# Kernel tuning notes

Measured on AMD Instinct MI355X. Metric: run time of the kernel, lower is better.

The kernel has to match this reference:

```python
import jax, jax.numpy as jnp
import numpy as np

D_IN = 2
D_Q = 8
N_TOKEN = 512
FPD = 64            # fre_per_dim = (N_TOKEN*D_Q)**(1/D_IN)
FRE_UB = 10.0
FFN_MULT = 4
N_ATTN = 4
N_MLP = 2           # n_total_blocks - n_attn_blocks
B = 8192
EPS_LN = 1e-5
EPS_SIG = 1e-8


def _ln(x, g, b):
    m = jnp.mean(x, axis=-1, keepdims=True)
    v = jnp.var(x, axis=-1, keepdims=True)
    return (x - m) * jax.lax.rsqrt(v + EPS_LN) * g + b


def _rff_buffers():
    # freqs: linspace(0, fre_ub, FPD+1)[1:]
    f = jnp.linspace(0.0, FRE_UB, FPD + 1)[1:]
    # cartesian_prod(f, f): first factor varies slowest
    grid = jnp.stack(jnp.meshgrid(f, f, indexing='ij'), axis=-1).reshape(-1, D_IN)
    omega_raw = grid.reshape(N_TOKEN, D_Q, D_IN)
    G = omega_raw[..., -1]                                 # [T, d_q]
    f_min = G.min(axis=-1, keepdims=True)
    f_max = G.max(axis=-1, keepdims=True)
    G = (G - f_min) / (f_max - f_min + EPS_SIG) * 2.0 - 1.0
    omega = omega_raw * jnp.sqrt(jnp.asarray(2.0 / (D_Q * N_TOKEN), jnp.float32))
    phase = jnp.linspace(0.0, 2.0 * np.pi, N_TOKEN * D_Q).reshape(1, N_TOKEN, D_Q)
    return omega.astype(jnp.float32), G.astype(jnp.float32), phase.astype(jnp.float32)


def setup_inputs() -> dict:
    key = jax.random.key(0)
    ks = iter(jax.random.split(key, 64))
    T, F = N_TOKEN, FFN_MULT * N_TOKEN
    s = 0.02

    def w(shape):
        return (jax.random.normal(next(ks), shape, jnp.float32) * s)

    omega, G, phase = _rff_buffers()
    inp = {
        'x': jax.random.normal(next(ks), (B, D_IN), jnp.float32),
        'omega': omega, 'G': G, 'phase': phase,
        'l1_w': w((T, D_IN)), 'l1_b': jnp.zeros((T,), jnp.float32),
        # attention blocks (stacked over N_ATTN)
        'mu_w': w((N_ATTN, T, T)), 'mu_b': jnp.zeros((N_ATTN, T), jnp.float32),
        'sg_w': w((N_ATTN, T, T)), 'sg_b': jnp.zeros((N_ATTN, T), jnp.float32),
        'aln_q_g': jnp.ones((N_ATTN, T), jnp.float32), 'aln_q_b': jnp.zeros((N_ATTN, T), jnp.float32),
        'aln_f_g': jnp.ones((N_ATTN, T), jnp.float32), 'aln_f_b': jnp.zeros((N_ATTN, T), jnp.float32),
        'a_w1': w((N_ATTN, F, T)), 'a_b1': jnp.zeros((N_ATTN, F), jnp.float32),
        'a_w2': w((N_ATTN, T, F)), 'a_b2': jnp.zeros((N_ATTN, T), jnp.float32),
        # MLP blocks (stacked over N_MLP)
        'mln_g': jnp.ones((N_MLP, T), jnp.float32), 'mln_b': jnp.zeros((N_MLP, T), jnp.float32),
        'm_w1': w((N_MLP, F, T)), 'm_b1': jnp.zeros((N_MLP, F), jnp.float32),
        'm_w2': w((N_MLP, T, F)), 'm_b2': jnp.zeros((N_MLP, T), jnp.float32),
        'ro_w': w((1, T)), 'ro_b': jnp.zeros((1,), jnp.float32),
    }
    return inp


def reference(x, omega, G, phase, l1_w, l1_b, mu_w, mu_b, sg_w, sg_b,
              aln_q_g, aln_q_b, aln_f_g, aln_f_b, a_w1, a_b1, a_w2, a_b2,
              mln_g, mln_b, m_w1, m_b1, m_w2, m_b2, ro_w, ro_b):
    # RFF tokenizer: H[b,n,k] = cos(omega[n,k,:] . x[b,:] + phase)
    H = jnp.cos(jnp.einsum('nkd,bd->bnk', omega, x) + phase)   # [B,T,d_q]
    Q = jax.nn.silu(x @ l1_w.T + l1_b)                          # [B,T]
    for i in range(N_ATTN):
        q = _ln(Q, aln_q_g[i], aln_q_b[i])
        mu = jnp.tanh(q @ mu_w[i].T + mu_b[i])[..., None]       # [B,T,1]
        sig = (q @ sg_w[i].T + sg_b[i])[..., None]              # [B,T,1]
        # Gaussian kernelized pseudo-attention; G broadcasts [T,d_q] -> [B,T,d_q]
        S = jnp.exp(-0.5 * (G - mu) ** 2 / (sig * sig + EPS_SIG))
        Q = Q + jnp.sum(S * H, axis=-1)
        h = _ln(Q, aln_f_g[i], aln_f_b[i])
        Q = Q + jax.nn.silu(h @ a_w1[i].T + a_b1[i]) @ a_w2[i].T + a_b2[i]
    for i in range(N_MLP):
        h = _ln(Q, mln_g[i], mln_b[i])
        Q = Q + jax.nn.silu(h @ m_w1[i].T + m_b1[i]) @ m_w2[i].T + m_b2[i]
    out = jax.nn.silu(Q) @ ro_w.T + ro_b                        # [B,1]
    return out[:, 0]
```

## Files before the change

kernel.cpp:

```cpp
#include <hip/hip_runtime.h>
#include <cmath>

namespace {

constexpr int BB = 8192;
constexpr int TT = 512;
constexpr int FF = 2048;
constexpr float EPS_LN  = 1e-5f;
constexpr float EPS_SIG = 1e-8f;

typedef _Float16 half8 __attribute__((ext_vector_type(8)));
typedef _Float16 half4 __attribute__((ext_vector_type(4)));
typedef float f32x4 __attribute__((ext_vector_type(4)));

typedef __attribute__((address_space(1))) void gvoid_t;
typedef __attribute__((address_space(3))) void lvoid_t;

__device__ __forceinline__ void async16(void* lds, const void* g) {
    __builtin_amdgcn_global_load_lds((gvoid_t*)g, (lvoid_t*)lds, 16, 0, 0);
}

__device__ __forceinline__ float silu_f(float v) {
    return v / (1.0f + expf(-v));
}
__device__ __forceinline__ float silu_fast(float v) {
    return v * __builtin_amdgcn_rcpf(1.0f + __expf(-v));
}

template <bool LO>
__global__ __launch_bounds__(256) void cvt_kernel(
    const float* __restrict__ s, _Float16* __restrict__ hi,
    _Float16* __restrict__ lo, int n) {
    int i = (blockIdx.x * 256 + threadIdx.x) * 4;
    if (i >= n) return;
    float4 v = *(const float4*)(s + i);
    half4 h;
    h[0] = (_Float16)v.x; h[1] = (_Float16)v.y;
    h[2] = (_Float16)v.z; h[3] = (_Float16)v.w;
    *(half4*)(hi + i) = h;
    if (LO) {
        half4 l;
        l[0] = (_Float16)(v.x - (float)h[0]);
        l[1] = (_Float16)(v.y - (float)h[1]);
        l[2] = (_Float16)(v.z - (float)h[2]);
        l[3] = (_Float16)(v.w - (float)h[3]);
        *(half4*)(lo + i) = l;
    }
}

__global__ __launch_bounds__(256) void cvtcat_kernel(
    const float* __restrict__ s, _Float16* __restrict__ hi,
    _Float16* __restrict__ lo, int base) {
    int i = (blockIdx.x * 256 + threadIdx.x) * 4;
    int dst = ((i >> 18) << 19) + base + (i & 262143);
    float4 v = *(const float4*)(s + i);
    half4 h, l;
    h[0] = (_Float16)v.x; h[1] = (_Float16)v.y;
    h[2] = (_Float16)v.z; h[3] = (_Float16)v.w;
    l[0] = (_Float16)(v.x - (float)h[0]);
    l[1] = (_Float16)(v.y - (float)h[1]);
    l[2] = (_Float16)(v.z - (float)h[2]);
    l[3] = (_Float16)(v.w - (float)h[3]);
    *(half4*)(hi + dst) = h;
    *(half4*)(lo + dst) = l;
}

__global__ __launch_bounds__(256) void tok_kernel(
    const float* __restrict__ x, const float* __restrict__ l1w,
    const float* __restrict__ l1b, float* __restrict__ Q) {
    int idx = blockIdx.x * 256 + threadIdx.x;
    int b = idx >> 9, t = idx & 511;
    float x0 = x[2 * b], x1 = x[2 * b + 1];
    float v = fmaf(x0, l1w[2 * t], fmaf(x1, l1w[2 * t + 1], l1b[t]));
    Q[idx] = silu_f(v);
}

template <bool LO>
__global__ __launch_bounds__(256) void ln_kernel(
    const float* __restrict__ X, const float* __restrict__ g,
    const float* __restrict__ bia, _Float16* __restrict__ Y,
    _Float16* __restrict__ Ylo) {
    int lane = threadIdx.x & 63;
    int row  = blockIdx.x * 4 + (threadIdx.x >> 6);
    const float* xr = X + (size_t)row * TT;
    float v[8];
    {
        float4 a = *(const float4*)(xr + lane * 8);
        float4 c = *(const float4*)(xr + lane * 8 + 4);
        v[0]=a.x; v[1]=a.y; v[2]=a.z; v[3]=a.w;
        v[4]=c.x; v[5]=c.y; v[6]=c.z; v[7]=c.w;
    }
    float s = 0.f;
    #pragma unroll
    for (int i = 0; i < 8; ++i) s += v[i];
    #pragma unroll
    for (int off = 32; off > 0; off >>= 1) s += __shfl_down(s, off);
    float mean = __shfl(s, 0) * (1.0f / TT);
    float ss = 0.f;
    #pragma unroll
    for (int i = 0; i < 8; ++i) { float d = v[i] - mean; ss = fmaf(d, d, ss); }
    #pragma unroll
    for (int off = 32; off > 0; off >>= 1) ss += __shfl_down(ss, off);
    float var  = __shfl(ss, 0) * (1.0f / TT);
    float rstd = rsqrtf(var + EPS_LN);
    half8 hv, lv;
    #pragma unroll
    for (int i = 0; i < 8; ++i) {
        int t = lane * 8 + i;
        float o = (v[i] - mean) * rstd * g[t] + bia[t];
        hv[i] = (_Float16)o;
        if (LO) lv[i] = (_Float16)(o - (float)hv[i]);
    }
    *(half8*)(Y + (size_t)row * TT + lane * 8) = hv;
    if (LO) *(half8*)(Ylo + (size_t)row * TT + lane * 8) = lv;
}

template <int BM, int BN, int WGM, int WGN, int NBUF, int MINW, bool SPLIT,
          int ACT, bool RESID, typename OutT>
__global__ __launch_bounds__(WGM * WGN * 64, MINW) void gemmdp_kernel(
    const _Float16* __restrict__ A, const _Float16* __restrict__ Alo,
    const _Float16* __restrict__ W, const _Float16* __restrict__ Wlo,
    const float* __restrict__ bias, const float* __restrict__ bias2,
    const float* __restrict__ R, OutT* __restrict__ C,
    int N, int K, int nsplit) {
    constexpr int BK      = 32;
    constexpr int THREADS = WGM * WGN * 64;
    constexpr int NS   = SPLIT ? 2 : 1;
    constexpr int D    = NBUF - 1;
    constexpr int CH_A = NS * BM * 4;
    constexpr int CH_T = NS * (BM + BN) * 4;
    constexpr int LPT  = CH_T / THREADS;
    static_assert(CH_T % THREADS == 0 && CH_A % THREADS == 0, "staging split");
    constexpr int ABUF = NS * BM * BK;
    constexpr int WBUF = NS * BN * BK;
    constexpr int WOFF = NBUF * ABUF;
    constexpr int WTM  = BM / WGM;
    constexpr int WTN  = BN / WGN;
    constexpr int MI   = WTM / 16;
    constexpr int NI   = WTN / 16;

    __shared__ alignas(16) _Float16 lds[NBUF * (ABUF + WBUF)];

    const int tid = threadIdx.x;
    const int m0  = blockIdx.x * BM;
    const int n0  = blockIdx.y * BN;

    const _Float16* Asrc[2] = {A, Alo};
    const _Float16* Wsrc[2] = {W, Wlo};

    const _Float16* gsrc[LPT];
    int off0[LPT], bstr[LPT];
    #pragma unroll
    for (int j = 0; j < LPT; ++j) {
        int idx = j * THREADS + tid;
        if (j * THREADS < CH_A) {
            int s   = idx / (BM * 4);
            int rc  = idx % (BM * 4);
            int row = rc >> 2, sl = rc & 3;
            int src = sl ^ ((row >> 1) & 3);
            gsrc[j] = Asrc[s] + (size_t)(m0 + row) * K + src * 8;
            off0[j] = (s * BM + row) * BK + sl * 8;
            bstr[j] = ABUF;
        } else {
            int i2  = idx - CH_A;
            int s   = i2 / (BN * 4);
            int rc  = i2 % (BN * 4);
            int row = rc >> 2, sl = rc & 3;
            int src = sl ^ ((row >> 1) & 3);
            gsrc[j] = Wsrc[s] + (size_t)(n0 + row) * K + src * 8;
            off0[j] = WOFF + (s * BN + row) * BK + sl * 8;
            bstr[j] = WBUF;
        }
    }

    auto stage = [&](int buf, int k0) {
        #pragma unroll
        for (int j = 0; j < LPT; ++j)
            async16(&lds[off0[j] + buf * bstr[j]], gsrc[j] + k0);
    };

    const int wid  = tid >> 6;
    const int wr   = wid / WGN;
    const int wc   = wid % WGN;
    const int lane = tid & 63;
    const int fr   = lane & 15;
    const int q    = lane >> 4;
    const int swz  = (q ^ ((fr >> 1) & 3)) * 8;

    const f32x4 vzero = {0.f, 0.f, 0.f, 0.f};
    f32x4 acc[MI][NI];
    #pragma unroll
    for (int mi = 0; mi < MI; ++mi)
        #pragma unroll
        for (int ni = 0; ni < NI; ++ni) acc[mi][ni] = vzero;

    auto body = [&](int buf) {
        const int da = buf * ABUF;
        const int dw = WOFF + buf * WBUF;
        half8 a[NS][MI], b[NS][NI];
        #pragma unroll
        for (int s = 0; s < NS; ++s) {
            #pragma unroll
            for (int mi = 0; mi < MI; ++mi)
                a[s][mi] = *(const half8*)&lds[da + (s * BM + wr * WTM + mi * 16 + fr) * BK + swz];
            #pragma unroll
            for (int ni = 0; ni < NI; ++ni)
                b[s][ni] = *(const half8*)&lds[dw + (s * BN + wc * WTN + ni * 16 + fr) * BK + swz];
        }
        __builtin_amdgcn_s_setprio(1);
        #pragma unroll
        for (int mi = 0; mi < MI; ++mi)
            #pragma unroll
            for (int ni = 0; ni < NI; ++ni)
                acc[mi][ni] = __builtin_amdgcn_mfma_f32_16x16x32_f16(
                    a[0][mi], b[0][ni], acc[mi][ni], 0, 0, 0);
        if (SPLIT) {
            #pragma unroll
            for (int mi = 0; mi < MI; ++mi)
                #pragma unroll
                for (int ni = 0; ni < NI; ++ni)
                    acc[mi][ni] = __builtin_amdgcn_mfma_f32_16x16x32_f16(
                        a[1][mi], b[0][ni], acc[mi][ni], 0, 0, 0);
            #pragma unroll
            for (int mi = 0; mi < MI; ++mi)
                #pragma unroll
                for (int ni = 0; ni < NI; ++ni)
                    acc[mi][ni] = __builtin_amdgcn_mfma_f32_16x16x32_f16(
                        a[0][mi], b[1][ni], acc[mi][ni], 0, 0, 0);
        }
        __builtin_amdgcn_s_setprio(0);
    };

    const int NK = K / BK;

    #pragma unroll
    for (int s = 0; s < D; ++s) stage(s, s * BK);

    int rbuf = 0, sbuf = D;
    for (int ki = 0; ki < NK - D; ++ki) {
        asm volatile("s_waitcnt vmcnt(%0)" :: "n"((D - 1) * LPT) : "memory");
        __builtin_amdgcn_s_barrier();
        asm volatile("" ::: "memory");
        stage(sbuf, (ki + D) * BK);
        sbuf = (sbuf + 1 == NBUF) ? 0 : sbuf + 1;
        body(rbuf);
        rbuf = (rbuf + 1 == NBUF) ? 0 : rbuf + 1;
    }
    if constexpr (D >= 3) {
        asm volatile("s_waitcnt vmcnt(%0)" :: "n"(2 * LPT) : "memory");
        __builtin_amdgcn_s_barrier();
        asm volatile("" ::: "memory");
        body(rbuf);
        rbuf = (rbuf + 1 == NBUF) ? 0 : rbuf + 1;
    }
    if constexpr (D >= 2) {
        asm volatile("s_waitcnt vmcnt(%0)" :: "n"(1 * LPT) : "memory");
        __builtin_amdgcn_s_barrier();
        asm volatile("" ::: "memory");
        body(rbuf);
        rbuf = (rbuf + 1 == NBUF) ? 0 : rbuf + 1;
    }
    asm volatile("s_waitcnt vmcnt(0)" ::: "memory");
    __builtin_amdgcn_s_barrier();
    asm volatile("" ::: "memory");
    body(rbuf);

    const bool fh = (n0 < nsplit);
    const float* bp = fh ? bias : bias2;
    const int coff = fh ? 0 : nsplit;
    const int r0 = q * 4;
    #pragma unroll
    for (int mi = 0; mi < MI; ++mi) {
        #pragma unroll
        for (int ni = 0; ni < NI; ++ni) {
            const int col = n0 + wc * WTN + ni * 16 + fr;
            const float bv = bp[col - coff];
            #pragma unroll
            for (int r = 0; r < 4; ++r) {
                const int row = m0 + wr * WTM + mi * 16 + r0 + r;
                float v = acc[mi][ni][r] + bv;
                if (ACT == 1) v = silu_fast(v);
                if (ACT == 3 && fh) v = tanhf(v);
                if (RESID) v += R[(size_t)row * N + col];
                C[(size_t)row * N + col] = (OutT)v;
            }
        }
    }
}

__global__ __launch_bounds__(512) void attnln_kernel(
    float* __restrict__ Q, const float* __restrict__ MS,
    const float* __restrict__ x,
    const float* __restrict__ omega, const float* __restrict__ G,
    const float* __restrict__ phase,
    const float* __restrict__ g, const float* __restrict__ bia,
    _Float16* __restrict__ Y) {
    __shared__ float cs[8][516];
    __shared__ float gs[8][516];
    __shared__ float red[2][8];
    const int tid = threadIdx.x;
    const int b   = blockIdx.x;
    const float x0 = x[2 * b], x1 = x[2 * b + 1];
    #pragma unroll
    for (int it = 0; it < 8; ++it) {
        int j = it * 512 + tid;
        float2 om = *(const float2*)(omega + 2 * j);
        float arg = fmaf(om.x, x0, fmaf(om.y, x1, phase[j]));
        cs[j & 7][j >> 3] = __cosf(arg);
        gs[j & 7][j >> 3] = G[j];
    }
    __syncthreads();
    const int t = tid;
    float mu  = MS[(size_t)b * 1024 + t];
    float sig = MS[(size_t)b * 1024 + 512 + t];
    float inv = -0.5f * __builtin_amdgcn_rcpf(fmaf(sig, sig, EPS_SIG));
    float acc = 0.f;
    #pragma unroll
    for (int k = 0; k < 8; ++k) {
        float d = gs[k][t] - mu;
        acc = fmaf(__expf(d * d * inv), cs[k][t], acc);
    }
    const size_t idx = (size_t)b * TT + t;
    float qn = Q[idx] + acc;
    Q[idx] = qn;
    const int wid = tid >> 6, lane = tid & 63;
    float s = qn;
    #pragma unroll
    for (int off = 32; off > 0; off >>= 1) s += __shfl_down(s, off);
    if (lane == 0) red[0][wid] = s;
    __syncthreads();
    float tot = 0.f;
    #pragma unroll
    for (int w = 0; w < 8; ++w) tot += red[0][w];
    float mean = tot * (1.0f / TT);
    float d = qn - mean;
    float ss = d * d;
    #pragma unroll
    for (int off = 32; off > 0; off >>= 1) ss += __shfl_down(ss, off);
    if (lane == 0) red[1][wid] = ss;
    __syncthreads();
    float vtot = 0.f;
    #pragma unroll
    for (int w = 0; w < 8; ++w) vtot += red[1][w];
    float rstd = rsqrtf(vtot * (1.0f / TT) + EPS_LN);
    Y[idx] = (_Float16)(d * rstd * g[t] + bia[t]);
}

__global__ __launch_bounds__(256) void readout_kernel(
    const float* __restrict__ Q, const float* __restrict__ row_,
    const float* __restrict__ rob, float* __restrict__ out) {
    int lane = threadIdx.x & 63;
    int row  = blockIdx.x * 4 + (threadIdx.x >> 6);
    const float* qr = Q + (size_t)row * TT;
    float acc = 0.f;
    #pragma unroll
    for (int i = 0; i < 8; ++i) {
        int t = lane * 8 + i;
        acc = fmaf(silu_f(qr[t]), row_[t], acc);
    }
    #pragma unroll
    for (int off = 32; off > 0; off >>= 1) acc += __shfl_down(acc, off);
    if (lane == 0) out[row] = acc + rob[0];
}

}

extern "C" void kernel_launch(void* const* d_in, const int* in_sizes, int n_in,
                              void* d_out, int out_size, void* d_ws, size_t ws_size,
                              hipStream_t stream) {
    const float* x     = (const float*)d_in[0];
    const float* omega = (const float*)d_in[1];
    const float* G     = (const float*)d_in[2];
    const float* phase = (const float*)d_in[3];
    const float* l1_w  = (const float*)d_in[4];
    const float* l1_b  = (const float*)d_in[5];
    const float* mu_w  = (const float*)d_in[6];
    const float* mu_b  = (const float*)d_in[7];
    const float* sg_w  = (const float*)d_in[8];
    const float* sg_b  = (const float*)d_in[9];
    const float* alqg  = (const float*)d_in[10];
    const float* alqb  = (const float*)d_in[11];
    const float* alfg  = (const float*)d_in[12];
    const float* alfb  = (const float*)d_in[13];
    const float* a_w1  = (const float*)d_in[14];
    const float* a_b1  = (const float*)d_in[15];
    const float* a_w2  = (const float*)d_in[16];
    const float* a_b2  = (const float*)d_in[17];
    const float* mln_g = (const float*)d_in[18];
    const float* mln_b = (const float*)d_in[19];
    const float* m_w1  = (const float*)d_in[20];
    const float* m_b1  = (const float*)d_in[21];
    const float* m_w2  = (const float*)d_in[22];
    const float* m_b2  = (const float*)d_in[23];
    const float* ro_w  = (const float*)d_in[24];
    const float* ro_b  = (const float*)d_in[25];

    char* ws = (char*)d_ws;
    float*     Q    = (float*)ws;
    _Float16*  h_hi = (_Float16*)(ws + 16777216);
    _Float16*  h_lo = (_Float16*)(ws + 25165824);
    _Float16*  mid  = (_Float16*)(ws + 33554432);
    float*     MS   = (float*)(ws + 33554432);
    _Float16*  wbuf = (_Float16*)(ws + 67108864);

    _Float16* msw_hi = wbuf;
    _Float16* msw_lo = msw_hi + 2097152;
    _Float16* aw1    = msw_lo + 2097152;
    _Float16* aw2    = aw1 + 4194304;
    _Float16* mw1    = aw2 + 4194304;
    _Float16* mw2    = mw1 + 2097152;

    dim3 blk(256);
    const int BIG = 1 << 30;

    cvtcat_kernel<<<1024, blk, 0, stream>>>(mu_w, msw_hi, msw_lo, 0);
    cvtcat_kernel<<<1024, blk, 0, stream>>>(sg_w, msw_hi, msw_lo, 262144);
    cvt_kernel<false><<<4096, blk, 0, stream>>>(a_w1, aw1, nullptr, 4194304);
    cvt_kernel<false><<<4096, blk, 0, stream>>>(a_w2, aw2, nullptr, 4194304);
    cvt_kernel<false><<<2048, blk, 0, stream>>>(m_w1, mw1, nullptr, 2097152);
    cvt_kernel<false><<<2048, blk, 0, stream>>>(m_w2, mw2, nullptr, 2097152);

    tok_kernel<<<BB * TT / 256, blk, 0, stream>>>(x, l1_w, l1_b, Q);

    for (int i = 0; i < 4; ++i) {
        ln_kernel<true><<<BB / 4, blk, 0, stream>>>(
            Q, alqg + i * TT, alqb + i * TT, h_hi, h_lo);
        gemmdp_kernel<256, 128, 4, 2, 3, 2, true, 3, false, float>
            <<<dim3(BB / 256, 1024 / 128), dim3(512), 0, stream>>>(
            h_hi, h_lo, msw_hi + (size_t)i * 524288, msw_lo + (size_t)i * 524288,
            mu_b + i * TT, sg_b + i * TT, nullptr, MS, 1024, TT, TT);
        attnln_kernel<<<BB, dim3(512), 0, stream>>>(
            Q, MS, x, omega, G, phase, alfg + i * TT, alfb + i * TT, h_hi);
        gemmdp_kernel<256, 128, 4, 2, 3, 4, false, 1, false, _Float16>
            <<<dim3(BB / 256, FF / 128), dim3(512), 0, stream>>>(
            h_hi, nullptr, aw1 + (size_t)i * 1048576, nullptr,
            a_b1 + i * FF, a_b1 + i * FF, nullptr, mid, FF, TT, BIG);
        gemmdp_kernel<128, 128, 2, 4, 4, 4, false, 0, true, float>
            <<<dim3(BB / 128, TT / 128), dim3(512), 0, stream>>>(
            mid, nullptr, aw2 + (size_t)i * 1048576, nullptr,
            a_b2 + i * TT, a_b2 + i * TT, Q, Q, TT, FF, BIG);
    }
    for (int i = 0; i < 2; ++i) {
        ln_kernel<false><<<BB / 4, blk, 0, stream>>>(
            Q, mln_g + i * TT, mln_b + i * TT, h_hi, nullptr);
        gemmdp_kernel<256, 128, 4, 2, 3, 4, false, 1, false, _Float16>
            <<<dim3(BB / 256, FF / 128), dim3(512), 0, stream>>>(
            h_hi, nullptr, mw1 + (size_t)i * 1048576, nullptr,
            m_b1 + i * FF, m_b1 + i * FF, nullptr, mid, FF, TT, BIG);
        gemmdp_kernel<128, 128, 2, 4, 4, 4, false, 0, true, float>
            <<<dim3(BB / 128, TT / 128), dim3(512), 0, stream>>>(
            mid, nullptr, mw2 + (size_t)i * 1048576, nullptr,
            m_b2 + i * TT, m_b2 + i * TT, Q, Q, TT, FF, BIG);
    }

    readout_kernel<<<BB / 4, blk, 0, stream>>>(Q, ro_w, ro_b, (float*)d_out);
}
```

Before: 766.8 us.

## Merge weight conversions, fuse tokenizer with first LN, add BK=64 GEMM tiles

All six weight-conversion launches become one kernel, and the tokenizer is fused with the first attention LayerNorm, so the first ln_kernel launch and one pass over Q are skipped. The GEMM kernel gains a templated BK. The up-projection GEMMs move to BK=64 with fewer waves per CU, and the down-projection GEMMs use a 5-deep buffer pipeline with an extra drain stage. The aim is fewer launches and barriers per K step, at the cost of more LDS use and lower occupancy.

```diff
diff --git a/kernel.cpp b/kernel.cpp
--- a/kernel.cpp
+++ b/kernel.cpp
@@ -27,52 +27,78 @@
     return v * __builtin_amdgcn_rcpf(1.0f + __expf(-v));
 }
 
-template <bool LO>
-__global__ __launch_bounds__(256) void cvt_kernel(
-    const float* __restrict__ s, _Float16* __restrict__ hi,
-    _Float16* __restrict__ lo, int n) {
+__global__ __launch_bounds__(256) void cvtall_kernel(
+    const float* __restrict__ mu_w, const float* __restrict__ sg_w,
+    const float* __restrict__ a_w1, const float* __restrict__ a_w2,
+    const float* __restrict__ m_w1, const float* __restrict__ m_w2,
+    _Float16* __restrict__ msw_hi, _Float16* __restrict__ msw_lo,
+    _Float16* __restrict__ aw1, _Float16* __restrict__ aw2,
+    _Float16* __restrict__ mw1, _Float16* __restrict__ mw2) {
     int i = (blockIdx.x * 256 + threadIdx.x) * 4;
-    if (i >= n) return;
-    float4 v = *(const float4*)(s + i);
-    half4 h;
-    h[0] = (_Float16)v.x; h[1] = (_Float16)v.y;
-    h[2] = (_Float16)v.z; h[3] = (_Float16)v.w;
-    *(half4*)(hi + i) = h;
-    if (LO) {
-        half4 l;
+    if (i < 2097152) {
+        const float* s; int base, ii = i;
+        if (i < 1048576) { s = mu_w; base = 0; }
+        else             { s = sg_w; base = 262144; ii -= 1048576; }
+        int dst = ((ii >> 18) << 19) + base + (ii & 262143);
+        float4 v = *(const float4*)(s + ii);
+        half4 h, l;
+        h[0] = (_Float16)v.x; h[1] = (_Float16)v.y;
+        h[2] = (_Float16)v.z; h[3] = (_Float16)v.w;
         l[0] = (_Float16)(v.x - (float)h[0]);
         l[1] = (_Float16)(v.y - (float)h[1]);
         l[2] = (_Float16)(v.z - (float)h[2]);
         l[3] = (_Float16)(v.w - (float)h[3]);
-        *(half4*)(lo + i) = l;
-    }
-}
-
-__global__ __launch_bounds__(256) void cvtcat_kernel(
-    const float* __restrict__ s, _Float16* __restrict__ hi,
-    _Float16* __restrict__ lo, int base) {
-    int i = (blockIdx.x * 256 + threadIdx.x) * 4;
-    int dst = ((i >> 18) << 19) + base + (i & 262143);
-    float4 v = *(const float4*)(s + i);
-    half4 h, l;
+        *(half4*)(msw_hi + dst) = h;
+        *(half4*)(msw_lo + dst) = l;
+        return;
+    }
+    const float* s; _Float16* d; int ii;
+    if      (i <  6291456) { s = a_w1; d = aw1; ii = i -  2097152; }
+    else if (i < 10485760) { s = a_w2; d = aw2; ii = i -  6291456; }
+    else if (i < 12582912) { s = m_w1; d = mw1; ii = i - 10485760; }
+    else                   { s = m_w2; d = mw2; ii = i - 12582912; }
+    float4 v = *(const float4*)(s + ii);
+    half4 h;
     h[0] = (_Float16)v.x; h[1] = (_Float16)v.y;
     h[2] = (_Float16)v.z; h[3] = (_Float16)v.w;
-    l[0] = (_Float16)(v.x - (float)h[0]);
-    l[1] = (_Float16)(v.y - (float)h[1]);
-    l[2] = (_Float16)(v.z - (float)h[2]);
-    l[3] = (_Float16)(v.w - (float)h[3]);
-    *(half4*)(hi + dst) = h;
-    *(half4*)(lo + dst) = l;
-}
-
-__global__ __launch_bounds__(256) void tok_kernel(
+    *(half4*)(d + ii) = h;
+}
+
+__global__ __launch_bounds__(512) void tokln_kernel(
     const float* __restrict__ x, const float* __restrict__ l1w,
-    const float* __restrict__ l1b, float* __restrict__ Q) {
-    int idx = blockIdx.x * 256 + threadIdx.x;
-    int b = idx >> 9, t = idx & 511;
-    float x0 = x[2 * b], x1 = x[2 * b + 1];
-    float v = fmaf(x0, l1w[2 * t], fmaf(x1, l1w[2 * t + 1], l1b[t]));
-    Q[idx] = silu_f(v);
+    const float* __restrict__ l1b,
+    const float* __restrict__ g, const float* __restrict__ bia,
+    float* __restrict__ Q, _Float16* __restrict__ Y, _Float16* __restrict__ Ylo) {
+    __shared__ float red[2][8];
+    const int tid = threadIdx.x, b = blockIdx.x, t = tid;
+    const float x0 = x[2 * b], x1 = x[2 * b + 1];
+    float qn = silu_f(fmaf(x0, l1w[2 * t], fmaf(x1, l1w[2 * t + 1], l1b[t])));
+    const size_t idx = (size_t)b * TT + t;
+    Q[idx] = qn;
+    const int wid = tid >> 6, lane = tid & 63;
+    float s = qn;
+    #pragma unroll
+    for (int off = 32; off > 0; off >>= 1) s += __shfl_down(s, off);
+    if (lane == 0) red[0][wid] = s;
+    __syncthreads();
+    float tot = 0.f;
+    #pragma unroll
+    for (int w = 0; w < 8; ++w) tot += red[0][w];
+    float mean = tot * (1.0f / TT);
+    float d = qn - mean;
+    float ss = d * d;
+    #pragma unroll
+    for (int off = 32; off > 0; off >>= 1) ss += __shfl_down(ss, off);
+    if (lane == 0) red[1][wid] = ss;
+    __syncthreads();
+    float vtot = 0.f;
+    #pragma unroll
+    for (int w = 0; w < 8; ++w) vtot += red[1][w];
+    float rstd = rsqrtf(vtot * (1.0f / TT) + EPS_LN);
+    float o = d * rstd * g[t] + bia[t];
+    _Float16 hv = (_Float16)o;
+    Y[idx] = hv;
+    Ylo[idx] = (_Float16)(o - (float)hv);
 }
 
 template <bool LO>
@@ -115,20 +141,20 @@
     if (LO) *(half8*)(Ylo + (size_t)row * TT + lane * 8) = lv;
 }
 
-template <int BM, int BN, int WGM, int WGN, int NBUF, int MINW, bool SPLIT,
-          int ACT, bool RESID, typename OutT>
+template <int BM, int BN, int BK, int WGM, int WGN, int NBUF, int MINW,
+          bool SPLIT, int ACT, bool RESID, typename OutT>
 __global__ __launch_bounds__(WGM * WGN * 64, MINW) void gemmdp_kernel(
     const _Float16* __restrict__ A, const _Float16* __restrict__ Alo,
     const _Float16* __restrict__ W, const _Float16* __restrict__ Wlo,
     const float* __restrict__ bias, const float* __restrict__ bias2,
     const float* __restrict__ R, OutT* __restrict__ C,
     int N, int K, int nsplit) {
-    constexpr int BK      = 32;
     constexpr int THREADS = WGM * WGN * 64;
+    constexpr int CPR  = BK / 8;
     constexpr int NS   = SPLIT ? 2 : 1;
     constexpr int D    = NBUF - 1;
-    constexpr int CH_A = NS * BM * 4;
-    constexpr int CH_T = NS * (BM + BN) * 4;
+    constexpr int CH_A = NS * BM * CPR;
+    constexpr int CH_T = NS * (BM + BN) * CPR;
     constexpr int LPT  = CH_T / THREADS;
     static_assert(CH_T % THREADS == 0 && CH_A % THREADS == 0, "staging split");
     constexpr int ABUF = NS * BM * BK;
@@ -154,19 +180,19 @@
     for (int j = 0; j < LPT; ++j) {
         int idx = j * THREADS + tid;
         if (j * THREADS < CH_A) {
-            int s   = idx / (BM * 4);
-            int rc  = idx % (BM * 4);
-            int row = rc >> 2, sl = rc & 3;
-            int src = sl ^ ((row >> 1) & 3);
+            int s   = idx / (BM * CPR);
+            int rc  = idx % (BM * CPR);
+            int row = rc / CPR, sl = rc % CPR;
+            int src = sl ^ ((row >> 1) & (CPR - 1));
             gsrc[j] = Asrc[s] + (size_t)(m0 + row) * K + src * 8;
             off0[j] = (s * BM + row) * BK + sl * 8;
             bstr[j] = ABUF;
         } else {
             int i2  = idx - CH_A;
-            int s   = i2 / (BN * 4);
-            int rc  = i2 % (BN * 4);
-            int row = rc >> 2, sl = rc & 3;
-            int src = sl ^ ((row >> 1) & 3);
+            int s   = i2 / (BN * CPR);
+            int rc  = i2 % (BN * CPR);
+            int row = rc / CPR, sl = rc % CPR;
+            int src = sl ^ ((row >> 1) & (CPR - 1));
             gsrc[j] = Wsrc[s] + (size_t)(n0 + row) * K + src * 8;
             off0[j] = WOFF + (s * BN + row) * BK + sl * 8;
             bstr[j] = WBUF;
@@ -185,7 +211,7 @@
     const int lane = tid & 63;
     const int fr   = lane & 15;
     const int q    = lane >> 4;
-    const int swz  = (q ^ ((fr >> 1) & 3)) * 8;
+    const int hxor = (fr >> 1) & (CPR - 1);
 
     const f32x4 vzero = {0.f, 0.f, 0.f, 0.f};
     f32x4 acc[MI][NI];
@@ -197,38 +223,42 @@
     auto body = [&](int buf) {
         const int da = buf * ABUF;
         const int dw = WOFF + buf * WBUF;
-        half8 a[NS][MI], b[NS][NI];
         #pragma unroll
-        for (int s = 0; s < NS; ++s) {
+        for (int ks = 0; ks < BK / 32; ++ks) {
+            const int swz = ((ks * 4 + q) ^ hxor) * 8;
+            half8 a[NS][MI], b[NS][NI];
             #pragma unroll
-            for (int mi = 0; mi < MI; ++mi)
-                a[s][mi] = *(const half8*)&lds[da + (s * BM + wr * WTM + mi * 16 + fr) * BK + swz];
-            #pragma unroll
-            for (int ni = 0; ni < NI; ++ni)
-                b[s][ni] = *(const half8*)&lds[dw + (s * BN + wc * WTN + ni * 16 + fr) * BK + swz];
-        }
-        __builtin_amdgcn_s_setprio(1);
-        #pragma unroll
-        for (int mi = 0; mi < MI; ++mi)
-            #pragma unroll
-            for (int ni = 0; ni < NI; ++ni)
-                acc[mi][ni] = __builtin_amdgcn_mfma_f32_16x16x32_f16(
-                    a[0][mi], b[0][ni], acc[mi][ni], 0, 0, 0);
-        if (SPLIT) {
+            for (int s = 0; s < NS; ++s) {
+                #pragma unroll
+                for (int mi = 0; mi < MI; ++mi)
+                    a[s][mi] = *(const half8*)&lds[da + (s * BM + wr * WTM + mi * 16 + fr) * BK + swz];
+                #pragma unroll
+                for (int ni = 0; ni < NI; ++ni)
+                    b[s][ni] = *(const half8*)&lds[dw + (s * BN + wc * WTN + ni * 16 + fr) * BK + swz];
+            }
+            __builtin_amdgcn_s_setprio(1);
             #pragma unroll
             for (int mi = 0; mi < MI; ++mi)
                 #pragma unroll
                 for (int ni = 0; ni < NI; ++ni)
                     acc[mi][ni] = __builtin_amdgcn_mfma_f32_16x16x32_f16(
-                        a[1][mi], b[0][ni], acc[mi][ni], 0, 0, 0);
-            #pragma unroll
-            for (int mi = 0; mi < MI; ++mi)
+                        a[0][mi], b[0][ni], acc[mi][ni], 0, 0, 0);
+            if (SPLIT) {
                 #pragma unroll
-                for (int ni = 0; ni < NI; ++ni)
-                    acc[mi][ni] = __builtin_amdgcn_mfma_f32_16x16x32_f16(
-                        a[0][mi], b[1][ni], acc[mi][ni], 0, 0, 0);
+                for (int mi = 0; mi < MI; ++mi)
+                    #pragma unroll
+                    for (int ni = 0; ni < NI; ++ni)
+                        acc[mi][ni] = __builtin_amdgcn_mfma_f32_16x16x32_f16(
+                            a[1][mi], b[0][ni], acc[mi][ni], 0, 0, 0);
+                #pragma unroll
+                for (int mi = 0; mi < MI; ++mi)
+                    #pragma unroll
+                    for (int ni = 0; ni < NI; ++ni)
+                        acc[mi][ni] = __builtin_amdgcn_mfma_f32_16x16x32_f16(
+                            a[0][mi], b[1][ni], acc[mi][ni], 0, 0, 0);
+            }
+            __builtin_amdgcn_s_setprio(0);
         }
-        __builtin_amdgcn_s_setprio(0);
     };
 
     const int NK = K / BK;
@@ -243,6 +273,13 @@
         asm volatile("" ::: "memory");
         stage(sbuf, (ki + D) * BK);
         sbuf = (sbuf + 1 == NBUF) ? 0 : sbuf + 1;
+        body(rbuf);
+        rbuf = (rbuf + 1 == NBUF) ? 0 : rbuf + 1;
+    }
+    if constexpr (D >= 4) {
+        asm volatile("s_waitcnt vmcnt(%0)" :: "n"(3 * LPT) : "memory");
+        __builtin_amdgcn_s_barrier();
+        asm volatile("" ::: "memory");
         body(rbuf);
         rbuf = (rbuf + 1 == NBUF) ? 0 : rbuf + 1;
     }
@@ -413,29 +450,28 @@
     dim3 blk(256);
     const int BIG = 1 << 30;
 
-    cvtcat_kernel<<<1024, blk, 0, stream>>>(mu_w, msw_hi, msw_lo, 0);
-    cvtcat_kernel<<<1024, blk, 0, stream>>>(sg_w, msw_hi, msw_lo, 262144);
-    cvt_kernel<false><<<4096, blk, 0, stream>>>(a_w1, aw1, nullptr, 4194304);
-    cvt_kernel<false><<<4096, blk, 0, stream>>>(a_w2, aw2, nullptr, 4194304);
-    cvt_kernel<false><<<2048, blk, 0, stream>>>(m_w1, mw1, nullptr, 2097152);
-    cvt_kernel<false><<<2048, blk, 0, stream>>>(m_w2, mw2, nullptr, 2097152);
-
-    tok_kernel<<<BB * TT / 256, blk, 0, stream>>>(x, l1_w, l1_b, Q);
+    cvtall_kernel<<<14336, blk, 0, stream>>>(
+        mu_w, sg_w, a_w1, a_w2, m_w1, m_w2,
+        msw_hi, msw_lo, aw1, aw2, mw1, mw2);
+
+    tokln_kernel<<<BB, dim3(512), 0, stream>>>(
+        x, l1_w, l1_b, alqg, alqb, Q, h_hi, h_lo);
 
     for (int i = 0; i < 4; ++i) {
-        ln_kernel<true><<<BB / 4, blk, 0, stream>>>(
-            Q, alqg + i * TT, alqb + i * TT, h_hi, h_lo);
-        gemmdp_kernel<256, 128, 4, 2, 3, 2, true, 3, false, float>
+        if (i > 0)
+            ln_kernel<true><<<BB / 4, blk, 0, stream>>>(
+                Q, alqg + i * TT, alqb + i * TT, h_hi, h_lo);
+        gemmdp_kernel<256, 128, 32, 4, 2, 3, 2, true, 3, false, float>
             <<<dim3(BB / 256, 1024 / 128), dim3(512), 0, stream>>>(
             h_hi, h_lo, msw_hi + (size_t)i * 524288, msw_lo + (size_t)i * 524288,
             mu_b + i * TT, sg_b + i * TT, nullptr, MS, 1024, TT, TT);
         attnln_kernel<<<BB, dim3(512), 0, stream>>>(
             Q, MS, x, omega, G, phase, alfg + i * TT, alfb + i * TT, h_hi);
-        gemmdp_kernel<256, 128, 4, 2, 3, 4, false, 1, false, _Float16>
+        gemmdp_kernel<256, 128, 64, 4, 2, 3, 2, false, 1, false, _Float16>
             <<<dim3(BB / 256, FF / 128), dim3(512), 0, stream>>>(
             h_hi, nullptr, aw1 + (size_t)i * 1048576, nullptr,
             a_b1 + i * FF, a_b1 + i * FF, nullptr, mid, FF, TT, BIG);
-        gemmdp_kernel<128, 128, 2, 4, 4, 4, false, 0, true, float>
+        gemmdp_kernel<128, 128, 32, 2, 4, 5, 4, false, 0, true, float>
             <<<dim3(BB / 128, TT / 128), dim3(512), 0, stream>>>(
             mid, nullptr, aw2 + (size_t)i * 1048576, nullptr,
             a_b2 + i * TT, a_b2 + i * TT, Q, Q, TT, FF, BIG);
@@ -443,11 +479,11 @@
     for (int i = 0; i < 2; ++i) {
         ln_kernel<false><<<BB / 4, blk, 0, stream>>>(
             Q, mln_g + i * TT, mln_b + i * TT, h_hi, nullptr);
-        gemmdp_kernel<256, 128, 4, 2, 3, 4, false, 1, false, _Float16>
+        gemmdp_kernel<256, 128, 64, 4, 2, 3, 2, false, 1, false, _Float16>
             <<<dim3(BB / 256, FF / 128), dim3(512), 0, stream>>>(
             h_hi, nullptr, mw1 + (size_t)i * 1048576, nullptr,
             m_b1 + i * FF, m_b1 + i * FF, nullptr, mid, FF, TT, BIG);
-        gemmdp_kernel<128, 128, 2, 4, 4, 4, false, 0, true, float>
+        gemmdp_kernel<128, 128, 32, 2, 4, 5, 4, false, 0, true, float>
             <<<dim3(BB / 128, TT / 128), dim3(512), 0, stream>>>(
             mid, nullptr, mw2 + (size_t)i * 1048576, nullptr,
             m_b2 + i * TT, m_b2 + i * TT, Q, Q, TT, FF, BIG);
```

After: 778.1 us. Within noise of the previous version (+1.5%).
